# Performance work log

Hardware: AMD Instinct MI355X
Metric: run time of the kernel (lower is better)

## Reference

```python
import jax, jax.numpy as jnp
import numpy as np

OUT = 7            # output_size
SR = 2             # sampling_ratio
SCALES = (0.25, 0.125, 0.0625, 0.03125)   # FPN strides 4,8,16,32
K_MIN, K_MAX = 2, 5
CANON_SCALE = 224.0
CANON_LVL = 4.0
EPS = 1e-6


def setup_inputs() -> dict:
    key = jax.random.key(0)
    ks = jax.random.split(key, 7)
    feat0 = jax.random.normal(ks[0], (2, 256, 200, 200), dtype=jnp.float32)
    feat1 = jax.random.normal(ks[1], (2, 256, 100, 100), dtype=jnp.float32)
    feat2 = jax.random.normal(ks[2], (2, 256, 50, 50), dtype=jnp.float32)
    feat3 = jax.random.normal(ks[3], (2, 256, 25, 25), dtype=jnp.float32)
    # boxes in 800x800 image coords: x1,y1 in [0,600), w,h in [2,200)
    xy = jax.random.uniform(ks[4], (2, 512, 2), dtype=jnp.float32) * 600.0
    wh = jax.random.uniform(ks[5], (2, 512, 2), dtype=jnp.float32) * 198.0 + 2.0
    boxes = jnp.concatenate([xy, xy + wh], axis=-1)  # [B,K,4] x1,y1,x2,y2
    return {"feat0": feat0, "feat1": feat1, "feat2": feat2, "feat3": feat3, "boxes": boxes}


def _bilinear(feat, bidx, ys, xs):
    # feat [B,C,H,W], bidx [N] int, ys [N,OY], xs [N,OX] -> [N,C,OY,OX]
    H, W = feat.shape[2], feat.shape[3]
    vy = (ys >= -1.0) & (ys <= float(H))
    vx = (xs >= -1.0) & (xs <= float(W))
    y = jnp.clip(ys, 0.0, H - 1.0)
    x = jnp.clip(xs, 0.0, W - 1.0)
    y0 = jnp.floor(y).astype(jnp.int32)
    x0 = jnp.floor(x).astype(jnp.int32)
    y1 = jnp.minimum(y0 + 1, H - 1)
    x1 = jnp.minimum(x0 + 1, W - 1)
    ly = y - y0
    lx = x - x0

    def g(yi, xi):
        # advanced indexing -> [N,OY,OX,C]
        return feat[bidx[:, None, None], :, yi[:, :, None], xi[:, None, :]]

    wy0 = (1.0 - ly)[:, :, None, None]
    wy1 = ly[:, :, None, None]
    wx0 = (1.0 - lx)[:, None, :, None]
    wx1 = lx[:, None, :, None]
    v = (wy0 * (wx0 * g(y0, x0) + wx1 * g(y0, x1))
         + wy1 * (wx0 * g(y1, x0) + wx1 * g(y1, x1)))
    v = v * (vy[:, :, None] & vx[:, None, :])[..., None].astype(v.dtype)
    return jnp.transpose(v, (0, 3, 1, 2))  # [N,C,OY,OX]


def _roi_align(feat, bidx, boxes, scale):
    # torchvision roi_align, aligned=False
    x1 = boxes[:, 0] * scale
    y1 = boxes[:, 1] * scale
    x2 = boxes[:, 2] * scale
    y2 = boxes[:, 3] * scale
    rw = jnp.maximum(x2 - x1, 1.0)
    rh = jnp.maximum(y2 - y1, 1.0)
    bw = rw / OUT
    bh = rh / OUT
    # flattened sample offsets: (j + 0.5)/SR in bin units, j in [0, OUT*SR)
    off = (jnp.arange(OUT * SR, dtype=jnp.float32) + 0.5) / SR
    ys = y1[:, None] + off[None, :] * bh[:, None]   # [N, OUT*SR]
    xs = x1[:, None] + off[None, :] * bw[:, None]   # [N, OUT*SR]
    v = _bilinear(feat, bidx, ys, xs)               # [N,C,OUT*SR,OUT*SR]
    N, C = v.shape[0], v.shape[1]
    v = v.reshape(N, C, OUT, SR, OUT, SR)
    return v.mean(axis=(3, 5))                      # [N,C,OUT,OUT]


def reference(feat0, feat1, feat2, feat3, boxes):
    feats = [feat0, feat1, feat2, feat3]
    B, K = boxes.shape[0], boxes.shape[1]
    boxes_f = boxes.reshape(-1, 4)                   # [N,4]
    bidx = jnp.repeat(jnp.arange(B, dtype=jnp.int32), K)
    # FPN level assignment (torchvision LevelMapper)
    area = (boxes_f[:, 2] - boxes_f[:, 0]) * (boxes_f[:, 3] - boxes_f[:, 1])
    lvl = jnp.floor(CANON_LVL + jnp.log2(jnp.sqrt(area) / CANON_SCALE + EPS))
    lvl = jnp.clip(lvl, K_MIN, K_MAX)
    idx = (lvl - K_MIN).astype(jnp.int32)            # [N] in {0..3}
    # compute ROI align at every level, select per box (jit-friendly)
    out = _roi_align(feats[0], bidx, boxes_f, SCALES[0])
    for l in range(1, 4):
        vl = _roi_align(feats[l], bidx, boxes_f, SCALES[l])
        out = jnp.where((idx == l)[:, None, None, None], vl, out)
    return out  # [B*K, C, 7, 7]
```

## Files before the change

### kernel.cpp

```cpp
#include <hip/hip_runtime.h>
#include <math.h>


constexpr int CH = 256;
constexpr int POUT = 7;
constexpr int NSAMP = 14;
constexpr int NBIN = POUT * POUT;
constexpr int PER_ROI = CH * NBIN;
constexpr int NWAVE = 2;
constexpr int CPW = 16;
constexpr int CPB = NWAVE * CPW;
constexpr int NCG = CH / CPB;

struct F2 { float x, y; };
__device__ inline F2 ld2(const float* p) { F2 v; __builtin_memcpy(&v, p, 8); return v; }
struct F4 { float x, y, z, w; };
__device__ inline F4 ld4(const float* p) { F4 v; __builtin_memcpy(&v, p, 16); return v; }

__global__ __launch_bounds__(128)
void roi_align_bin3_kernel(const float* __restrict__ f0,
                           const float* __restrict__ f1,
                           const float* __restrict__ f2,
                           const float* __restrict__ f3,
                           const float* __restrict__ boxes,
                           float* __restrict__ out,
                           int K)
{
    __shared__ int   s_rowoff[2 * NSAMP];
    __shared__ float s_wy0[NSAMP], s_wy1[NSAMP];
    __shared__ int   s_xlc[NSAMP];
    __shared__ float s_ex0[NSAMP], s_ex1[NSAMP];

    const int tid  = threadIdx.x;
    const int wave = tid >> 6;
    const int lane = tid & 63;
    const int roi  = blockIdx.x >> 3;
    const int cg   = blockIdx.x & (NCG - 1);
    const int b    = roi / K;

    const float bx1 = boxes[roi * 4 + 0], by1 = boxes[roi * 4 + 1];
    const float bx2 = boxes[roi * 4 + 2], by2 = boxes[roi * 4 + 3];

    const float area = (bx2 - bx1) * (by2 - by1);
    float lvlf = floorf(4.0f + log2f(sqrtf(area) / 224.0f + 1e-6f));
    lvlf = fminf(fmaxf(lvlf, 2.0f), 5.0f);
    const int lvl = (int)lvlf - 2;

    const float* feat; int H, W; float scale;
    if (lvl == 0)      { feat = f0; H = 200; W = 200; scale = 0.25f;    }
    else if (lvl == 1) { feat = f1; H = 100; W = 100; scale = 0.125f;   }
    else if (lvl == 2) { feat = f2; H = 50;  W = 50;  scale = 0.0625f;  }
    else               { feat = f3; H = 25;  W = 25;  scale = 0.03125f; }

    const float x1 = bx1 * scale, y1 = by1 * scale;
    const float rw = fmaxf(bx2 * scale - x1, 1.0f);
    const float rh = fmaxf(by2 * scale - y1, 1.0f);
    const float bw = rw * (1.0f / POUT);
    const float bh = rh * (1.0f / POUT);

    if (tid < 2 * NSAMP) {
        const bool isY = tid < NSAMP;
        const int i = isY ? tid : tid - NSAMP;
        const float dim   = isY ? (float)H : (float)W;
        const float start = isY ? y1 : x1;
        const float bsz   = isY ? bh : bw;
        const float p = start + ((float)i + 0.5f) * 0.5f * bsz;
        const float valid = (p >= -1.0f && p <= dim) ? 1.0f : 0.0f;
        const float pc = fminf(fmaxf(p, 0.0f), dim - 1.0f);
        const int q0 = (int)floorf(pc);
        const float l = pc - (float)q0;
        const float w0 = (1.0f - l) * valid;
        const float w1 = l * valid;
        if (isY) {
            const int q1 = min(q0 + 1, (int)dim - 1);
            s_rowoff[2 * i]     = q0 * W;
            s_rowoff[2 * i + 1] = q1 * W;
            s_wy0[i] = w0 * 0.25f;
            s_wy1[i] = w1 * 0.25f;
        } else {
            const bool edge = (q0 > W - 2);
            s_xlc[i] = edge ? (W - 2) : q0;
            s_ex0[i] = edge ? 0.0f : w0;
            s_ex1[i] = edge ? (w1 + w0) : w1;
        }
    }
    __syncthreads();

    bool narrow = true;
    #pragma unroll
    for (int j = 0; j < POUT; ++j)
        narrow = narrow && (s_xlc[2 * j + 1] - s_xlc[2 * j] <= 2);

    const int  lp = (lane < NBIN) ? lane : (NBIN - 1);
    const bool act = (lane < NBIN);
    const int  by = lp / POUT, bx = lp - POUT * by;

    const int ro0 = s_rowoff[4 * by + 0];
    const int ro1 = s_rowoff[4 * by + 1];
    const int ro2 = s_rowoff[4 * by + 2];
    const int ro3 = s_rowoff[4 * by + 3];
    const float wy0 = s_wy0[2 * by],     wy1 = s_wy1[2 * by];
    const float wy2 = s_wy0[2 * by + 1], wy3 = s_wy1[2 * by + 1];

    const int lc0 = s_xlc[2 * bx], lc1 = s_xlc[2 * bx + 1];
    const float e00 = s_ex0[2 * bx],     e01 = s_ex1[2 * bx];
    const float e10 = s_ex0[2 * bx + 1], e11 = s_ex1[2 * bx + 1];

    const int HW = H * W;
    const int cbase = cg * CPB + wave * CPW;
    const float* chan0 = feat + ((size_t)b * CH + cbase) * (size_t)HW;
    const size_t obase = (size_t)roi * PER_ROI + (size_t)cbase * NBIN + lp;

    if (narrow) {
        const int base = min(lc0, W - 4);
        const int i0 = lc0 - base;
        const int i1 = lc1 - base;
        const float w40 = (i0 == 0 ? e00 : 0.0f) + (i1 == 0 ? e10 : 0.0f);
        const float w41 = (i0 == 1 ? e00 : 0.0f) + (i0 == 0 ? e01 : 0.0f)
                        + (i1 == 1 ? e10 : 0.0f) + (i1 == 0 ? e11 : 0.0f);
        const float w42 = (i0 == 2 ? e00 : 0.0f) + (i0 == 1 ? e01 : 0.0f)
                        + (i1 == 2 ? e10 : 0.0f) + (i1 == 1 ? e11 : 0.0f);
        const float w43 = (i0 == 2 ? e01 : 0.0f) + (i1 == 2 ? e11 : 0.0f);

        F4 v0 = ld4(chan0 + ro0 + base);
        F4 v1 = ld4(chan0 + ro1 + base);
        F4 v2 = ld4(chan0 + ro2 + base);
        F4 v3 = ld4(chan0 + ro3 + base);

        #pragma unroll
        for (int c = 0; c < CPW; ++c) {
            F4 n0, n1, n2, n3;
            if (c + 1 < CPW) {
                const float* ch = chan0 + (size_t)(c + 1) * HW;
                n0 = ld4(ch + ro0 + base);
                n1 = ld4(ch + ro1 + base);
                n2 = ld4(ch + ro2 + base);
                n3 = ld4(ch + ro3 + base);
            }
            const float rv0 = v0.x * w40 + v0.y * w41 + v0.z * w42 + v0.w * w43;
            const float rv1 = v1.x * w40 + v1.y * w41 + v1.z * w42 + v1.w * w43;
            const float rv2 = v2.x * w40 + v2.y * w41 + v2.z * w42 + v2.w * w43;
            const float rv3 = v3.x * w40 + v3.y * w41 + v3.z * w42 + v3.w * w43;
            const float acc = wy0 * rv0 + wy1 * rv1 + wy2 * rv2 + wy3 * rv3;
            if (act) out[obase + (size_t)c * NBIN] = acc;
            v0 = n0; v1 = n1; v2 = n2; v3 = n3;
        }
    } else {
        F2 a0 = ld2(chan0 + ro0 + lc0), d0 = ld2(chan0 + ro0 + lc1);
        F2 a1 = ld2(chan0 + ro1 + lc0), d1 = ld2(chan0 + ro1 + lc1);
        F2 a2 = ld2(chan0 + ro2 + lc0), d2 = ld2(chan0 + ro2 + lc1);
        F2 a3 = ld2(chan0 + ro3 + lc0), d3 = ld2(chan0 + ro3 + lc1);

        #pragma unroll
        for (int c = 0; c < CPW; ++c) {
            F2 na0, na1, na2, na3, nd0, nd1, nd2, nd3;
            if (c + 1 < CPW) {
                const float* ch = chan0 + (size_t)(c + 1) * HW;
                na0 = ld2(ch + ro0 + lc0); nd0 = ld2(ch + ro0 + lc1);
                na1 = ld2(ch + ro1 + lc0); nd1 = ld2(ch + ro1 + lc1);
                na2 = ld2(ch + ro2 + lc0); nd2 = ld2(ch + ro2 + lc1);
                na3 = ld2(ch + ro3 + lc0); nd3 = ld2(ch + ro3 + lc1);
            }
            const float rv0 = e00 * a0.x + e01 * a0.y + e10 * d0.x + e11 * d0.y;
            const float rv1 = e00 * a1.x + e01 * a1.y + e10 * d1.x + e11 * d1.y;
            const float rv2 = e00 * a2.x + e01 * a2.y + e10 * d2.x + e11 * d2.y;
            const float rv3 = e00 * a3.x + e01 * a3.y + e10 * d3.x + e11 * d3.y;
            const float acc = wy0 * rv0 + wy1 * rv1 + wy2 * rv2 + wy3 * rv3;
            if (act) out[obase + (size_t)c * NBIN] = acc;
            a0 = na0; a1 = na1; a2 = na2; a3 = na3;
            d0 = nd0; d1 = nd1; d2 = nd2; d3 = nd3;
        }
    }
}

extern "C" void kernel_launch(void* const* d_in, const int* in_sizes, int n_in,
                              void* d_out, int out_size, void* d_ws, size_t ws_size,
                              hipStream_t stream) {
    const float* f0    = (const float*)d_in[0];
    const float* f1    = (const float*)d_in[1];
    const float* f2    = (const float*)d_in[2];
    const float* f3    = (const float*)d_in[3];
    const float* boxes = (const float*)d_in[4];
    float* out = (float*)d_out;

    const int B    = in_sizes[0] / (256 * 200 * 200);
    const int nroi = in_sizes[4] / 4;
    const int K    = nroi / B;

    roi_align_bin3_kernel<<<nroi * NCG, 128, 0, stream>>>(f0, f1, f2, f3, boxes, out, K);
}
```

Measured before the change: 64.93 us.

## Use single-wave blocks with 8 channels and deeper multi-buffered load pipeline

Switches from 128-thread blocks handling 32 channels to 64-thread single-wave blocks handling 8 channels each, quadrupling the grid. With one wave per block, __syncthreads is replaced by an LDS waitcnt plus a scheduling barrier. The per-channel loop becomes a manually pipelined sequence with triple buffering (narrow path) or double buffering (wide path), so more loads are in flight per wave. The cost is more blocks that each recompute the box and level setup, and higher register use per wave.

Measured after the change: 70.30 us. 8.3% more time.

```diff
diff --git a/kernel.cpp b/kernel.cpp
--- a/kernel.cpp
+++ b/kernel.cpp
@@ -7,34 +7,30 @@
 constexpr int NSAMP = 14;
 constexpr int NBIN = POUT * POUT;
 constexpr int PER_ROI = CH * NBIN;
-constexpr int NWAVE = 2;
-constexpr int CPW = 16;
-constexpr int CPB = NWAVE * CPW;
-constexpr int NCG = CH / CPB;
+constexpr int CPW = 8;
+constexpr int NCG = CH / CPW;
 
 struct F2 { float x, y; };
 __device__ inline F2 ld2(const float* p) { F2 v; __builtin_memcpy(&v, p, 8); return v; }
 struct F4 { float x, y, z, w; };
 __device__ inline F4 ld4(const float* p) { F4 v; __builtin_memcpy(&v, p, 16); return v; }
 
-__global__ __launch_bounds__(128)
-void roi_align_bin3_kernel(const float* __restrict__ f0,
-                           const float* __restrict__ f1,
-                           const float* __restrict__ f2,
-                           const float* __restrict__ f3,
-                           const float* __restrict__ boxes,
-                           float* __restrict__ out,
-                           int K)
+__global__ __launch_bounds__(64, 7)
+void roi_align_mlp_kernel(const float* __restrict__ f0,
+                          const float* __restrict__ f1,
+                          const float* __restrict__ f2,
+                          const float* __restrict__ f3,
+                          const float* __restrict__ boxes,
+                          float* __restrict__ out,
+                          int K)
 {
     __shared__ int   s_rowoff[2 * NSAMP];
     __shared__ float s_wy0[NSAMP], s_wy1[NSAMP];
     __shared__ int   s_xlc[NSAMP];
     __shared__ float s_ex0[NSAMP], s_ex1[NSAMP];
 
-    const int tid  = threadIdx.x;
-    const int wave = tid >> 6;
-    const int lane = tid & 63;
-    const int roi  = blockIdx.x >> 3;
+    const int lane = threadIdx.x;
+    const int roi  = blockIdx.x >> 5;
     const int cg   = blockIdx.x & (NCG - 1);
     const int b    = roi / K;
 
@@ -58,9 +54,9 @@
     const float bw = rw * (1.0f / POUT);
     const float bh = rh * (1.0f / POUT);
 
-    if (tid < 2 * NSAMP) {
-        const bool isY = tid < NSAMP;
-        const int i = isY ? tid : tid - NSAMP;
+    if (lane < 2 * NSAMP) {
+        const bool isY = lane < NSAMP;
+        const int i = isY ? lane : lane - NSAMP;
         const float dim   = isY ? (float)H : (float)W;
         const float start = isY ? y1 : x1;
         const float bsz   = isY ? bh : bw;
@@ -84,7 +80,8 @@
             s_ex1[i] = edge ? (w1 + w0) : w1;
         }
     }
-    __syncthreads();
+    asm volatile("s_waitcnt lgkmcnt(0)" ::: "memory");
+    __builtin_amdgcn_sched_barrier(0);
 
     bool narrow = true;
     #pragma unroll
@@ -107,7 +104,7 @@
     const float e10 = s_ex0[2 * bx + 1], e11 = s_ex1[2 * bx + 1];
 
     const int HW = H * W;
-    const int cbase = cg * CPB + wave * CPW;
+    const int cbase = cg * CPW;
     const float* chan0 = feat + ((size_t)b * CH + cbase) * (size_t)HW;
     const size_t obase = (size_t)roi * PER_ROI + (size_t)cbase * NBIN + lp;
 
@@ -122,54 +119,71 @@
                         + (i1 == 2 ? e10 : 0.0f) + (i1 == 1 ? e11 : 0.0f);
         const float w43 = (i0 == 2 ? e01 : 0.0f) + (i1 == 2 ? e11 : 0.0f);
 
-        F4 v0 = ld4(chan0 + ro0 + base);
-        F4 v1 = ld4(chan0 + ro1 + base);
-        F4 v2 = ld4(chan0 + ro2 + base);
-        F4 v3 = ld4(chan0 + ro3 + base);
-
-        #pragma unroll
-        for (int c = 0; c < CPW; ++c) {
-            F4 n0, n1, n2, n3;
-            if (c + 1 < CPW) {
-                const float* ch = chan0 + (size_t)(c + 1) * HW;
-                n0 = ld4(ch + ro0 + base);
-                n1 = ld4(ch + ro1 + base);
-                n2 = ld4(ch + ro2 + base);
-                n3 = ld4(ch + ro3 + base);
-            }
-            const float rv0 = v0.x * w40 + v0.y * w41 + v0.z * w42 + v0.w * w43;
-            const float rv1 = v1.x * w40 + v1.y * w41 + v1.z * w42 + v1.w * w43;
-            const float rv2 = v2.x * w40 + v2.y * w41 + v2.z * w42 + v2.w * w43;
-            const float rv3 = v3.x * w40 + v3.y * w41 + v3.z * w42 + v3.w * w43;
-            const float acc = wy0 * rv0 + wy1 * rv1 + wy2 * rv2 + wy3 * rv3;
-            if (act) out[obase + (size_t)c * NBIN] = acc;
-            v0 = n0; v1 = n1; v2 = n2; v3 = n3;
-        }
+        F4 A0, A1, A2, A3, B0, B1, B2, B3, C0, C1, C2, C3;
+
+#define LDN(S0, S1, S2, S3, c) do {                                            \
+    const float* ch_ = chan0 + (size_t)(c) * HW;                               \
+    S0 = ld4(ch_ + ro0 + base);                                                \
+    S1 = ld4(ch_ + ro1 + base);                                                \
+    S2 = ld4(ch_ + ro2 + base);                                                \
+    S3 = ld4(ch_ + ro3 + base);                                                \
+} while (0)
+
+#define CPN(S0, S1, S2, S3, c) do {                                            \
+    const float rv0 = S0.x * w40 + S0.y * w41 + S0.z * w42 + S0.w * w43;       \
+    const float rv1 = S1.x * w40 + S1.y * w41 + S1.z * w42 + S1.w * w43;       \
+    const float rv2 = S2.x * w40 + S2.y * w41 + S2.z * w42 + S2.w * w43;       \
+    const float rv3 = S3.x * w40 + S3.y * w41 + S3.z * w42 + S3.w * w43;       \
+    const float acc = wy0 * rv0 + wy1 * rv1 + wy2 * rv2 + wy3 * rv3;           \
+    if (act) out[obase + (size_t)(c) * NBIN] = acc;                            \
+} while (0)
+
+        LDN(A0, A1, A2, A3, 0);
+        LDN(B0, B1, B2, B3, 1);
+        LDN(C0, C1, C2, C3, 2);
+        CPN(A0, A1, A2, A3, 0); LDN(A0, A1, A2, A3, 3);
+        CPN(B0, B1, B2, B3, 1); LDN(B0, B1, B2, B3, 4);
+        CPN(C0, C1, C2, C3, 2); LDN(C0, C1, C2, C3, 5);
+        CPN(A0, A1, A2, A3, 3); LDN(A0, A1, A2, A3, 6);
+        CPN(B0, B1, B2, B3, 4); LDN(B0, B1, B2, B3, 7);
+        CPN(C0, C1, C2, C3, 5);
+        CPN(A0, A1, A2, A3, 6);
+        CPN(B0, B1, B2, B3, 7);
+#undef LDN
+#undef CPN
     } else {
-        F2 a0 = ld2(chan0 + ro0 + lc0), d0 = ld2(chan0 + ro0 + lc1);
-        F2 a1 = ld2(chan0 + ro1 + lc0), d1 = ld2(chan0 + ro1 + lc1);
-        F2 a2 = ld2(chan0 + ro2 + lc0), d2 = ld2(chan0 + ro2 + lc1);
-        F2 a3 = ld2(chan0 + ro3 + lc0), d3 = ld2(chan0 + ro3 + lc1);
-
-        #pragma unroll
-        for (int c = 0; c < CPW; ++c) {
-            F2 na0, na1, na2, na3, nd0, nd1, nd2, nd3;
-            if (c + 1 < CPW) {
-                const float* ch = chan0 + (size_t)(c + 1) * HW;
-                na0 = ld2(ch + ro0 + lc0); nd0 = ld2(ch + ro0 + lc1);
-                na1 = ld2(ch + ro1 + lc0); nd1 = ld2(ch + ro1 + lc1);
-                na2 = ld2(ch + ro2 + lc0); nd2 = ld2(ch + ro2 + lc1);
-                na3 = ld2(ch + ro3 + lc0); nd3 = ld2(ch + ro3 + lc1);
-            }
-            const float rv0 = e00 * a0.x + e01 * a0.y + e10 * d0.x + e11 * d0.y;
-            const float rv1 = e00 * a1.x + e01 * a1.y + e10 * d1.x + e11 * d1.y;
-            const float rv2 = e00 * a2.x + e01 * a2.y + e10 * d2.x + e11 * d2.y;
-            const float rv3 = e00 * a3.x + e01 * a3.y + e10 * d3.x + e11 * d3.y;
-            const float acc = wy0 * rv0 + wy1 * rv1 + wy2 * rv2 + wy3 * rv3;
-            if (act) out[obase + (size_t)c * NBIN] = acc;
-            a0 = na0; a1 = na1; a2 = na2; a3 = na3;
-            d0 = nd0; d1 = nd1; d2 = nd2; d3 = nd3;
-        }
+        F2 a0, a1, a2, a3, d0, d1, d2, d3;
+        F2 p0, p1, p2, p3, q0, q1, q2, q3;
+
+#define LDW(Sa0, Sa1, Sa2, Sa3, Sd0, Sd1, Sd2, Sd3, c) do {                    \
+    const float* ch_ = chan0 + (size_t)(c) * HW;                               \
+    Sa0 = ld2(ch_ + ro0 + lc0); Sd0 = ld2(ch_ + ro0 + lc1);                    \
+    Sa1 = ld2(ch_ + ro1 + lc0); Sd1 = ld2(ch_ + ro1 + lc1);                    \
+    Sa2 = ld2(ch_ + ro2 + lc0); Sd2 = ld2(ch_ + ro2 + lc1);                    \
+    Sa3 = ld2(ch_ + ro3 + lc0); Sd3 = ld2(ch_ + ro3 + lc1);                    \
+} while (0)
+
+#define CPW_(Sa0, Sa1, Sa2, Sa3, Sd0, Sd1, Sd2, Sd3, c) do {                   \
+    const float rv0 = e00 * Sa0.x + e01 * Sa0.y + e10 * Sd0.x + e11 * Sd0.y;   \
+    const float rv1 = e00 * Sa1.x + e01 * Sa1.y + e10 * Sd1.x + e11 * Sd1.y;   \
+    const float rv2 = e00 * Sa2.x + e01 * Sa2.y + e10 * Sd2.x + e11 * Sd2.y;   \
+    const float rv3 = e00 * Sa3.x + e01 * Sa3.y + e10 * Sd3.x + e11 * Sd3.y;   \
+    const float acc = wy0 * rv0 + wy1 * rv1 + wy2 * rv2 + wy3 * rv3;           \
+    if (act) out[obase + (size_t)(c) * NBIN] = acc;                            \
+} while (0)
+
+        LDW(a0, a1, a2, a3, d0, d1, d2, d3, 0);
+        LDW(p0, p1, p2, p3, q0, q1, q2, q3, 1);
+        CPW_(a0, a1, a2, a3, d0, d1, d2, d3, 0); LDW(a0, a1, a2, a3, d0, d1, d2, d3, 2);
+        CPW_(p0, p1, p2, p3, q0, q1, q2, q3, 1); LDW(p0, p1, p2, p3, q0, q1, q2, q3, 3);
+        CPW_(a0, a1, a2, a3, d0, d1, d2, d3, 2); LDW(a0, a1, a2, a3, d0, d1, d2, d3, 4);
+        CPW_(p0, p1, p2, p3, q0, q1, q2, q3, 3); LDW(p0, p1, p2, p3, q0, q1, q2, q3, 5);
+        CPW_(a0, a1, a2, a3, d0, d1, d2, d3, 4); LDW(a0, a1, a2, a3, d0, d1, d2, d3, 6);
+        CPW_(p0, p1, p2, p3, q0, q1, q2, q3, 5); LDW(p0, p1, p2, p3, q0, q1, q2, q3, 7);
+        CPW_(a0, a1, a2, a3, d0, d1, d2, d3, 6);
+        CPW_(p0, p1, p2, p3, q0, q1, q2, q3, 7);
+#undef LDW
+#undef CPW_
     }
 }
 
@@ -187,5 +201,5 @@
     const int nroi = in_sizes[4] / 4;
     const int K    = nroi / B;
 
-    roi_align_bin3_kernel<<<nroi * NCG, 128, 0, stream>>>(f0, f1, f2, f3, boxes, out, K);
+    roi_align_mlp_kernel<<<nroi * NCG, 64, 0, stream>>>(f0, f1, f2, f3, boxes, out, K);
 }
```
